# Performance work log

Hardware: AMD Instinct MI355X
Metric: run time of the kernel (lower is better)

The kernel has to match this reference:

```python
import jax, jax.numpy as jnp
import numpy as np

N, E = 50000, 800000
DIN, DH, DOUT, L = 128, 256, 64, 4


def setup_inputs() -> dict:
    key = jax.random.key(0)
    ks = jax.random.split(key, 8)
    x = jax.random.normal(ks[0], (N, DIN), dtype=jnp.float32)
    edge_index = jax.random.randint(ks[1], (2, E), 0, N, dtype=jnp.int64 if jax.config.jax_enable_x64 else jnp.int32)
    W_emb = jax.random.normal(ks[2], (DIN, DH), dtype=jnp.float32) / np.float32(np.sqrt(DIN))
    b_emb = jnp.zeros((DH,), jnp.float32)
    W_conv = jax.random.normal(ks[3], (L, DH, DH), dtype=jnp.float32) / np.float32(np.sqrt(DH))
    b_conv = jnp.zeros((L, DH), jnp.float32)
    W_out = jax.random.normal(ks[4], (DH, DOUT), dtype=jnp.float32) / np.float32(np.sqrt(DH))
    b_out = jnp.zeros((DOUT,), jnp.float32)
    return {"x": x, "edge_index": edge_index, "W_emb": W_emb, "b_emb": b_emb,
            "W_conv": W_conv, "b_conv": b_conv, "W_out": W_out, "b_out": b_out}


def _gcn_layer(h, src, dst, norm, W, b, n):
    # GCNConv: transform, then sym-normalized neighbor aggregation, then bias
    h = h @ W                                  # [N, DH]
    msg = h[src] * norm[:, None]               # [E+N, DH] gather + scale
    return jax.ops.segment_sum(msg, dst, num_segments=n) + b


def reference(x, edge_index, W_emb, b_emb, W_conv, b_conv, W_out, b_out):
    n = x.shape[0]
    loop = jnp.arange(n, dtype=edge_index.dtype)
    src = jnp.concatenate([edge_index[0], loop])   # add self-loops (PyG default)
    dst = jnp.concatenate([edge_index[1], loop])
    deg = jax.ops.segment_sum(jnp.ones_like(src, dtype=x.dtype), dst, num_segments=n)
    dinv = jnp.where(deg > 0, jax.lax.rsqrt(deg), jnp.zeros_like(deg))
    norm = dinv[src] * dinv[dst]                   # per-edge D^-1/2 A D^-1/2 weight
    h = x @ W_emb + b_emb                          # embedding (no activation)
    for i in range(L):                             # small fixed layer count
        h = jnp.tanh(_gcn_layer(h, src, dst, norm, W_conv[i], b_conv[i], n))
    return h @ W_out + b_out
```

## Files before the change

### kernel.cpp

```cpp
#include <hip/hip_runtime.h>
#include <math.h>

#define N_NODES 50000
#define N_EDGES 800000
#define DIN 128
#define DH 256
#define DOUT 64
#define NLAYERS 4

typedef unsigned short u16;
typedef __attribute__((ext_vector_type(8))) _Float16 half8;
typedef __attribute__((ext_vector_type(4))) float f32x4;
typedef __attribute__((ext_vector_type(4), aligned(8))) int int4a;

__device__ inline u16 f2h(float f) {
  _Float16 h = (_Float16)f;
  return *(u16*)&h;
}
__device__ inline float h2f(u16 u) {
  _Float16 h = *(_Float16*)&u;
  return (float)h;
}
__device__ inline int invp(int j) {
  int s = j >> 6, t = j & 63;
  return s * 64 + (t & 3) * 16 + (t >> 2);
}

#define GLD16(gp, lp)                                                        \
  __builtin_amdgcn_global_load_lds(                                          \
      (const __attribute__((address_space(1))) void*)(const void*)(gp),      \
      (__attribute__((address_space(3))) void*)(void*)(lp), 16, 0, 0)


__global__ void k_scan1(const int* __restrict__ cnt, int* __restrict__ rowptr,
                        int* __restrict__ bsum, float* __restrict__ dinv, int n) {
  __shared__ int sm[256];
  int i = blockIdx.x * 256 + threadIdx.x;
  int v = (i < n) ? cnt[i] : 0;
  if (i < n) dinv[i] = rsqrtf((float)v + 1.0f);
  sm[threadIdx.x] = v;
  __syncthreads();
  for (int off = 1; off < 256; off <<= 1) {
    int t = (threadIdx.x >= off) ? sm[threadIdx.x - off] : 0;
    __syncthreads();
    sm[threadIdx.x] += t;
    __syncthreads();
  }
  if (i < n) rowptr[i + 1] = sm[threadIdx.x];
  if (threadIdx.x == 255) bsum[blockIdx.x] = sm[255];
}

__global__ void k_scan2(int* bsum, int nb) {
  __shared__ int sm[256];
  int v = (threadIdx.x < nb) ? bsum[threadIdx.x] : 0;
  sm[threadIdx.x] = v;
  __syncthreads();
  for (int off = 1; off < 256; off <<= 1) {
    int t = (threadIdx.x >= off) ? sm[threadIdx.x - off] : 0;
    __syncthreads();
    sm[threadIdx.x] += t;
    __syncthreads();
  }
  if (threadIdx.x < nb) bsum[threadIdx.x] = sm[threadIdx.x] - v;
}

__global__ void k_scan3(int* __restrict__ rowptr, const int* __restrict__ bsum,
                        int* __restrict__ cursor, int n) {
  int i = blockIdx.x * 256 + threadIdx.x;
  if (i < n) {
    int v = rowptr[i + 1] + bsum[blockIdx.x];
    rowptr[i + 1] = v;
    if (i + 1 < n) cursor[i + 1] = v;
  }
  if (blockIdx.x == 0 && threadIdx.x == 0) {
    rowptr[0] = 0;
    cursor[0] = 0;
  }
}

__global__ void k_fill(const int* __restrict__ src, const int* __restrict__ dst,
                       const float* __restrict__ dinv,
                       int* __restrict__ cursor, int2* __restrict__ csr, int e) {
  int i = blockIdx.x * blockDim.x + threadIdx.x;
  if (i < e) {
    int d = dst[i], s = src[i];
    int pos = atomicAdd(&cursor[d], 1);
    csr[pos] = make_int2(s, __float_as_int(dinv[s] * dinv[d]));
  }
}

#define X_Q (N_NODES * DIN / 4)
#define W_EMB_SZ (DIN * DH)
#define W_CONV_SZ (DH * DH)
#define W_OUT_SZ (3 * DH * DOUT)
#define W_TOT (W_EMB_SZ + 4 * W_CONV_SZ + W_OUT_SZ)
#define B_TOT (DH + 4 * DH)

__global__ void k_convert(const float* __restrict__ x, u16* __restrict__ x_f16,
                          const float* __restrict__ W_emb, const float* __restrict__ W_conv,
                          const float* __restrict__ W_out,
                          const float* __restrict__ b_emb, const float* __restrict__ b_conv,
                          u16* __restrict__ Bt_emb, u16* __restrict__ Bt_conv,
                          u16* __restrict__ Bt_out,
                          float* __restrict__ bEmbP, float* __restrict__ bConvP,
                          const int* __restrict__ edst, int* __restrict__ cnt) {
  int i = blockIdx.x * 256 + threadIdx.x;
  if (i < X_Q) {
    float4 v = ((const float4*)x)[i];
    ushort4 o;
    o.x = f2h(v.x); o.y = f2h(v.y); o.z = f2h(v.z); o.w = f2h(v.w);
    ((ushort4*)x_f16)[i] = o;
    return;
  }
  int t = i - X_Q;
  if (t < W_EMB_SZ) {
    int n = t >> 7, k = t & (DIN - 1);
    Bt_emb[t] = f2h(W_emb[k * DH + n]);
  } else if (t < W_EMB_SZ + 4 * W_CONV_SZ) {
    int j = t - W_EMB_SZ;
    int l = j >> 16, jj = j & (W_CONV_SZ - 1);
    int n = jj >> 8, k2 = jj & (DH - 1);
    Bt_conv[j] = f2h(W_conv[l * W_CONV_SZ + invp(k2) * DH + n]);
  } else if (t < W_TOT) {
    int j = t - W_EMB_SZ - 4 * W_CONV_SZ;
    int n = j / (3 * DH), kp = j % (3 * DH);
    int s0 = kp >> 8, k2 = kp & (DH - 1);
    float wv = W_out[invp(k2) * DOUT + n];
    u16 hiv = f2h(wv);
    u16 v = hiv;
    if (s0 == 1) v = f2h(wv - h2f(hiv));
    Bt_out[j] = v;
  } else {
    int t2 = t - W_TOT;
    if (t2 < B_TOT) {
      if (t2 < DH) bEmbP[t2] = b_emb[invp(t2)];
      else {
        int j = t2 - DH, l = j >> 8, jj = j & (DH - 1);
        bConvP[j] = b_conv[l * DH + invp(jj)];
      }
    } else {
      int t3 = t2 - B_TOT;
      if (t3 < N_EDGES) atomicAdd(&cnt[edst[t3]], 1);
    }
  }
}

template <int BN, int NSPLIT, int EPI>
__global__ __launch_bounds__(256) void k_gemm_mfma(
    const u16* __restrict__ Ahi, const u16* __restrict__ Alo,
    const u16* __restrict__ Bt, const float* __restrict__ bias,
    float* __restrict__ Cf, u16* __restrict__ Cb, int M, int K, int N) {
  constexpr int BM = 128, BK = 64;
  constexpr int WN = BN / 2;
  constexpr int NT = WN / 16;
  __shared__ u16 As[2 * 8 * 512];
  const int tid = threadIdx.x;
  const int w = tid >> 6, lane = tid & 63;
  const int q = lane >> 4, r = lane & 15;
  const int wmg = (w >> 1) * 4;
  const int wn = (w & 1) * WN;
  const int m0 = blockIdx.x * BM, n0 = blockIdx.y * BN;
  const int Kp = NSPLIT * K;
  const int srow = lane & 15;
  const int sk = (lane >> 4) * 8;

  f32x4 acc[4][NT];
#pragma unroll
  for (int t = 0; t < 4; t++)
#pragma unroll
    for (int u = 0; u < NT; u++) acc[t][u] = (f32x4){0.f, 0.f, 0.f, 0.f};

  for (int k0 = 0; k0 < Kp; k0 += BK) {
    const u16* Aptr;
    int ka;
    if (NSPLIT == 1) {
      Aptr = Ahi; ka = k0;
    } else {
      Aptr = (k0 < 2 * K) ? Ahi : Alo;
      ka = (k0 < K) ? k0 : ((k0 < 2 * K) ? (k0 - K) : (k0 - 2 * K));
    }
#pragma unroll
    for (int ii = 0; ii < 4; ii++) {
      int g = w * 2 + (ii & 1), kb = ii >> 1;
      int grow = m0 + g * 16 + srow;
      if (grow > M - 1) grow = M - 1;
      const u16* gp = Aptr + (size_t)grow * K + ka + kb * 32 + sk;
      GLD16(gp, &As[(kb * 8 + g) * 512] + (size_t)lane * 8);
    }
    __syncthreads();
#pragma unroll
    for (int kb = 0; kb < 2; kb++) {
      half8 af[4], bfr[NT];
#pragma unroll
      for (int u = 0; u < NT; u++)
        bfr[u] = *(const half8*)(Bt + (size_t)(n0 + wn + u * 16 + r) * Kp +
                                 k0 + kb * 32 + q * 8);
#pragma unroll
      for (int t = 0; t < 4; t++)
        af[t] = *(const half8*)&As[((kb * 8 + wmg + t) * 64 + lane) * 8];
#pragma unroll
      for (int t = 0; t < 4; t++)
#pragma unroll
        for (int u = 0; u < NT; u++)
          acc[t][u] = __builtin_amdgcn_mfma_f32_16x16x32_f16(af[t], bfr[u], acc[t][u], 0, 0, 0);
    }
    __syncthreads();
  }

  if (EPI == 1) {
    int cb = n0 + wn;
    float4 bp = bias ? *(const float4*)(bias + cb + r * 4)
                     : make_float4(0.f, 0.f, 0.f, 0.f);
#pragma unroll
    for (int t = 0; t < 4; t++) {
#pragma unroll
      for (int rg = 0; rg < 4; rg++) {
        int row = m0 + (w >> 1) * 64 + t * 16 + q * 4 + rg;
        if (row < M) {
          ushort4 o;
          o.x = f2h(acc[t][0][rg] + bp.x);
          o.y = f2h(acc[t][1][rg] + bp.y);
          o.z = f2h(acc[t][2][rg] + bp.z);
          o.w = f2h(acc[t][3][rg] + bp.w);
          *(ushort4*)(Cb + (size_t)row * N + cb + r * 4) = o;
        }
      }
    }
  } else {
    float bv[NT];
#pragma unroll
    for (int u = 0; u < NT; u++) bv[u] = bias ? bias[n0 + wn + u * 16 + r] : 0.f;
#pragma unroll
    for (int t = 0; t < 4; t++) {
#pragma unroll
      for (int rg = 0; rg < 4; rg++) {
        int row = m0 + (w >> 1) * 64 + t * 16 + q * 4 + rg;
        if (row < M) {
#pragma unroll
          for (int u = 0; u < NT; u++) {
            int col = n0 + wn + u * 16 + r;
            Cf[(size_t)row * N + col] = acc[t][u][rg] + bv[u];
          }
        }
      }
    }
  }
}

__global__ __launch_bounds__(256) void k_aggregate(
    const u16* __restrict__ tmph,
    const int* __restrict__ rowptr, const int2* __restrict__ csr,
    const float* __restrict__ dinv, const float* __restrict__ bias,
    u16* __restrict__ hi, u16* __restrict__ lo, int n) {
  int iw = (int)((blockIdx.x * (size_t)blockDim.x + threadIdx.x) >> 6);
  int i = __builtin_amdgcn_readfirstlane(iw);
  if (i >= n) return;
  int lane = threadIdx.x & 63;
  float w0 = dinv[i];
  w0 *= w0;
  const ushort4* T = (const ushort4*)tmph;
  float4 bv = ((const float4*)bias)[lane];
  int s = rowptr[i], e = rowptr[i + 1];
  ushort4 t0 = T[(size_t)i * 64 + lane];
  float ax = bv.x + w0 * h2f(t0.x);
  float ay = bv.y + w0 * h2f(t0.y);
  float az = bv.z + w0 * h2f(t0.z);
  float aw = bv.w + w0 * h2f(t0.w);
  int j = s;
  for (; j + 16 <= e; j += 16) {
    int4a q[8];
#pragma unroll
    for (int u = 0; u < 8; u++) q[u] = *(const int4a*)(csr + j + 2 * u);
    ushort4 v[16];
#pragma unroll
    for (int u = 0; u < 8; u++) {
      v[2 * u] = T[(size_t)q[u].x * 64 + lane];
      v[2 * u + 1] = T[(size_t)q[u].z * 64 + lane];
    }
#pragma unroll
    for (int u = 0; u < 8; u++) {
      float f0 = __int_as_float(q[u].y);
      ax += f0 * h2f(v[2 * u].x);
      ay += f0 * h2f(v[2 * u].y);
      az += f0 * h2f(v[2 * u].z);
      aw += f0 * h2f(v[2 * u].w);
      float f1 = __int_as_float(q[u].w);
      ax += f1 * h2f(v[2 * u + 1].x);
      ay += f1 * h2f(v[2 * u + 1].y);
      az += f1 * h2f(v[2 * u + 1].z);
      aw += f1 * h2f(v[2 * u + 1].w);
    }
  }
  if (j < e) {
    int2 c[16];
    float f[16];
    ushort4 v[16];
#pragma unroll
    for (int u = 0; u < 16; u++) {
      int idx = j + u;
      int cl = idx < e ? idx : e - 1;
      c[u] = csr[cl];
      f[u] = idx < e ? __int_as_float(c[u].y) : 0.f;
    }
#pragma unroll
    for (int u = 0; u < 16; u++) v[u] = T[(size_t)c[u].x * 64 + lane];
#pragma unroll
    for (int u = 0; u < 16; u++) {
      ax += f[u] * h2f(v[u].x);
      ay += f[u] * h2f(v[u].y);
      az += f[u] * h2f(v[u].z);
      aw += f[u] * h2f(v[u].w);
    }
  }
  float ox = tanhf(ax), oy = tanhf(ay), oz = tanhf(az), ow = tanhf(aw);
  size_t base = (size_t)i * DH + lane * 4;
  ushort4 hv;
  hv.x = f2h(ox); hv.y = f2h(oy); hv.z = f2h(oz); hv.w = f2h(ow);
  *(ushort4*)(hi + base) = hv;
  if (lo) {
    ushort4 lv;
    lv.x = f2h(ox - h2f(hv.x));
    lv.y = f2h(oy - h2f(hv.y));
    lv.z = f2h(oz - h2f(hv.z));
    lv.w = f2h(ow - h2f(hv.w));
    *(ushort4*)(lo + base) = lv;
  }
}


extern "C" void kernel_launch(void* const* d_in, const int* in_sizes, int n_in,
                              void* d_out, int out_size, void* d_ws, size_t ws_size,
                              hipStream_t stream) {
  const float* x = (const float*)d_in[0];
  const int* eidx = (const int*)d_in[1];
  const int* esrc = eidx;
  const int* edst = eidx + N_EDGES;
  const float* W_emb = (const float*)d_in[2];
  const float* b_emb = (const float*)d_in[3];
  const float* W_conv = (const float*)d_in[4];
  const float* b_conv = (const float*)d_in[5];
  const float* W_out = (const float*)d_in[6];
  const float* b_out = (const float*)d_in[7];
  float* out = (float*)d_out;

  char* ws = (char*)d_ws;
  size_t off = 0;
  auto alloc = [&](size_t bytes) -> void* {
    void* p = ws + off;
    off += (bytes + 255) & ~(size_t)255;
    return p;
  };
  u16* tmph = (u16*)alloc((size_t)N_NODES * DH * 2);
  u16* h_hi = (u16*)alloc((size_t)N_NODES * DH * 2);
  u16* h_lo = (u16*)alloc((size_t)N_NODES * DH * 2);
  u16* x_f16 = h_lo;
  float* dinv = (float*)alloc((size_t)N_NODES * 4);
  int* cnt = (int*)alloc((size_t)N_NODES * 4);
  int* rowptr = (int*)alloc((size_t)(N_NODES + 1) * 4);
  int* cursor = (int*)alloc((size_t)N_NODES * 4);
  int* bsum = (int*)alloc((size_t)((N_NODES + 255) / 256) * 4);
  int2* csr = (int2*)alloc((size_t)N_EDGES * 8);
  u16* Bt_emb = (u16*)alloc((size_t)W_EMB_SZ * 2);
  u16* Bt_conv = (u16*)alloc((size_t)4 * W_CONV_SZ * 2);
  u16* Bt_out = (u16*)alloc((size_t)W_OUT_SZ * 2);
  float* bEmbP = (float*)alloc((size_t)DH * 4);
  float* bConvP = (float*)alloc((size_t)4 * DH * 4);

  int nb = (N_NODES + 255) / 256;
  int eb = (N_EDGES + 255) / 256;

  hipMemsetAsync(cnt, 0, (size_t)N_NODES * 4, stream);
  {
    int tot = X_Q + W_TOT + B_TOT + N_EDGES;
    k_convert<<<(tot + 255) / 256, 256, 0, stream>>>(x, x_f16, W_emb, W_conv, W_out,
                                                     b_emb, b_conv, Bt_emb, Bt_conv,
                                                     Bt_out, bEmbP, bConvP, edst, cnt);
  }
  k_scan1<<<nb, 256, 0, stream>>>(cnt, rowptr, bsum, dinv, N_NODES);
  k_scan2<<<1, 256, 0, stream>>>(bsum, nb);
  k_scan3<<<nb, 256, 0, stream>>>(rowptr, bsum, cursor, N_NODES);
  k_fill<<<eb, 256, 0, stream>>>(esrc, edst, dinv, cursor, csr, N_EDGES);

  int mblocks = (N_NODES + 127) / 128;
  int aggblocks = (N_NODES * 64 + 255) / 256;

  {
    dim3 g(mblocks, DH / 128);
    k_gemm_mfma<128, 1, 1><<<g, 256, 0, stream>>>(x_f16, nullptr, Bt_emb, bEmbP,
                                                  nullptr, h_hi, N_NODES, DIN, DH);
  }
  for (int l = 0; l < NLAYERS; l++) {
    dim3 g(mblocks, DH / 128);
    k_gemm_mfma<128, 1, 1><<<g, 256, 0, stream>>>(h_hi, nullptr,
                                                  Bt_conv + (size_t)l * W_CONV_SZ, nullptr,
                                                  nullptr, tmph, N_NODES, DH, DH);
    k_aggregate<<<aggblocks, 256, 0, stream>>>(tmph, rowptr, csr, dinv,
                                               bConvP + (size_t)l * DH,
                                               h_hi, (l == 3) ? h_lo : nullptr, N_NODES);
  }
  {
    dim3 g(mblocks, 1);
    k_gemm_mfma<64, 3, 0><<<g, 256, 0, stream>>>(h_hi, h_lo, Bt_out, b_out,
                                                 out, nullptr, N_NODES, DH, DOUT);
  }
}
```

Before: 556.3 us.

## Split aggregation into feature slices with eight nodes per wave

The aggregation kernel is reorganized so each block handles one of eight 32-feature slices for 32 nodes. Each wave now processes eight nodes with eight lanes per node instead of one node per wave. This puts consecutive blocks on the same feature slice of the gather table, improving cache locality and giving more independent gathers per wave. CSR loads and output stores also become nontemporal. In exchange, each CSR entry is read once per slice (eight times in total), the unroll drops from 16 to 8, and lanes within a wave can diverge on uneven node degrees.

```diff
diff --git a/kernel.cpp b/kernel.cpp
--- a/kernel.cpp
+++ b/kernel.cpp
@@ -11,7 +11,8 @@
 typedef unsigned short u16;
 typedef __attribute__((ext_vector_type(8))) _Float16 half8;
 typedef __attribute__((ext_vector_type(4))) float f32x4;
-typedef __attribute__((ext_vector_type(4), aligned(8))) int int4a;
+typedef __attribute__((ext_vector_type(2))) int i32x2;
+typedef __attribute__((ext_vector_type(4))) unsigned short u16x4;
 
 __device__ inline u16 f2h(float f) {
   _Float16 h = (_Float16)f;
@@ -252,78 +253,76 @@
     const int* __restrict__ rowptr, const int2* __restrict__ csr,
     const float* __restrict__ dinv, const float* __restrict__ bias,
     u16* __restrict__ hi, u16* __restrict__ lo, int n) {
-  int iw = (int)((blockIdx.x * (size_t)blockDim.x + threadIdx.x) >> 6);
-  int i = __builtin_amdgcn_readfirstlane(iw);
+  const int slice = blockIdx.x & 7;
+  const int chunk = blockIdx.x >> 3;
+  const int lane = threadIdx.x & 63;
+  const int wave = threadIdx.x >> 6;
+  const int grp = lane >> 3, sub = lane & 7;
+  const int i = chunk * 32 + wave * 8 + grp;
   if (i >= n) return;
-  int lane = threadIdx.x & 63;
+  const int fo = slice * 32 + sub * 4;
+  const int col = slice * 8 + sub;
   float w0 = dinv[i];
   w0 *= w0;
-  const ushort4* T = (const ushort4*)tmph;
-  float4 bv = ((const float4*)bias)[lane];
+  const u16x4* T = (const u16x4*)tmph;
+  float4 bv = *(const float4*)(bias + fo);
+  u16x4 t0 = T[(size_t)i * 64 + col];
+  float ax = bv.x + w0 * h2f(t0[0]);
+  float ay = bv.y + w0 * h2f(t0[1]);
+  float az = bv.z + w0 * h2f(t0[2]);
+  float aw = bv.w + w0 * h2f(t0[3]);
   int s = rowptr[i], e = rowptr[i + 1];
-  ushort4 t0 = T[(size_t)i * 64 + lane];
-  float ax = bv.x + w0 * h2f(t0.x);
-  float ay = bv.y + w0 * h2f(t0.y);
-  float az = bv.z + w0 * h2f(t0.z);
-  float aw = bv.w + w0 * h2f(t0.w);
   int j = s;
-  for (; j + 16 <= e; j += 16) {
-    int4a q[8];
-#pragma unroll
-    for (int u = 0; u < 8; u++) q[u] = *(const int4a*)(csr + j + 2 * u);
-    ushort4 v[16];
+  for (; j + 8 <= e; j += 8) {
+    i32x2 c[8];
+    u16x4 v[8];
+#pragma unroll
+    for (int u = 0; u < 8; u++)
+      c[u] = __builtin_nontemporal_load((const i32x2*)(csr + j + u));
+#pragma unroll
+    for (int u = 0; u < 8; u++) v[u] = T[(size_t)c[u][0] * 64 + col];
 #pragma unroll
     for (int u = 0; u < 8; u++) {
-      v[2 * u] = T[(size_t)q[u].x * 64 + lane];
-      v[2 * u + 1] = T[(size_t)q[u].z * 64 + lane];
-    }
+      float f = __int_as_float(c[u][1]);
+      ax += f * h2f(v[u][0]);
+      ay += f * h2f(v[u][1]);
+      az += f * h2f(v[u][2]);
+      aw += f * h2f(v[u][3]);
+    }
+  }
+  if (j < e) {
+    i32x2 c[8];
+    float f[8];
+    u16x4 v[8];
 #pragma unroll
     for (int u = 0; u < 8; u++) {
-      float f0 = __int_as_float(q[u].y);
-      ax += f0 * h2f(v[2 * u].x);
-      ay += f0 * h2f(v[2 * u].y);
-      az += f0 * h2f(v[2 * u].z);
-      aw += f0 * h2f(v[2 * u].w);
-      float f1 = __int_as_float(q[u].w);
-      ax += f1 * h2f(v[2 * u + 1].x);
-      ay += f1 * h2f(v[2 * u + 1].y);
-      az += f1 * h2f(v[2 * u + 1].z);
-      aw += f1 * h2f(v[2 * u + 1].w);
-    }
-  }
-  if (j < e) {
-    int2 c[16];
-    float f[16];
-    ushort4 v[16];
-#pragma unroll
-    for (int u = 0; u < 16; u++) {
       int idx = j + u;
       int cl = idx < e ? idx : e - 1;
-      c[u] = csr[cl];
-      f[u] = idx < e ? __int_as_float(c[u].y) : 0.f;
-    }
-#pragma unroll
-    for (int u = 0; u < 16; u++) v[u] = T[(size_t)c[u].x * 64 + lane];
-#pragma unroll
-    for (int u = 0; u < 16; u++) {
-      ax += f[u] * h2f(v[u].x);
-      ay += f[u] * h2f(v[u].y);
-      az += f[u] * h2f(v[u].z);
-      aw += f[u] * h2f(v[u].w);
+      c[u] = __builtin_nontemporal_load((const i32x2*)(csr + cl));
+      f[u] = idx < e ? __int_as_float(c[u][1]) : 0.f;
+    }
+#pragma unroll
+    for (int u = 0; u < 8; u++) v[u] = T[(size_t)c[u][0] * 64 + col];
+#pragma unroll
+    for (int u = 0; u < 8; u++) {
+      ax += f[u] * h2f(v[u][0]);
+      ay += f[u] * h2f(v[u][1]);
+      az += f[u] * h2f(v[u][2]);
+      aw += f[u] * h2f(v[u][3]);
     }
   }
   float ox = tanhf(ax), oy = tanhf(ay), oz = tanhf(az), ow = tanhf(aw);
-  size_t base = (size_t)i * DH + lane * 4;
-  ushort4 hv;
-  hv.x = f2h(ox); hv.y = f2h(oy); hv.z = f2h(oz); hv.w = f2h(ow);
-  *(ushort4*)(hi + base) = hv;
+  size_t base = (size_t)i * DH + fo;
+  u16x4 hv;
+  hv[0] = f2h(ox); hv[1] = f2h(oy); hv[2] = f2h(oz); hv[3] = f2h(ow);
+  __builtin_nontemporal_store(hv, (u16x4*)(hi + base));
   if (lo) {
-    ushort4 lv;
-    lv.x = f2h(ox - h2f(hv.x));
-    lv.y = f2h(oy - h2f(hv.y));
-    lv.z = f2h(oz - h2f(hv.z));
-    lv.w = f2h(ow - h2f(hv.w));
-    *(ushort4*)(lo + base) = lv;
+    u16x4 lv;
+    lv[0] = f2h(ox - h2f(hv[0]));
+    lv[1] = f2h(oy - h2f(hv[1]));
+    lv[2] = f2h(oz - h2f(hv[2]));
+    lv[3] = f2h(ow - h2f(hv[3]));
+    __builtin_nontemporal_store(lv, (u16x4*)(lo + base));
   }
 }
 
@@ -382,7 +381,7 @@
   k_fill<<<eb, 256, 0, stream>>>(esrc, edst, dinv, cursor, csr, N_EDGES);
 
   int mblocks = (N_NODES + 127) / 128;
-  int aggblocks = (N_NODES * 64 + 255) / 256;
+  int aggblocks = ((N_NODES + 31) / 32) * 8;
 
   {
     dim3 g(mblocks, DH / 128);
```

Result: slower. 851.7 us (+53.1%).
